# Kernel tuning notes

Measured on AMD Instinct MI355X. Metric: run time of the kernel, lower is better.

Reference implementation:

```python
import jax, jax.numpy as jnp
import numpy as np

HEAD_SIZE = 64

def setup_inputs() -> dict:
    key = jax.random.key(0)
    kx, kk, kq, kv = jax.random.split(key, 4)
    B, T, C, H = 8, 2048, 1024, HEAD_SIZE
    scale = 1.0 / np.sqrt(C)
    x = jax.random.normal(kx, (B, T, C), dtype=jnp.float32)
    # nn.Linear(n_emb, head_size, bias=False) weights, shape (head_size, n_emb)
    Wk = jax.random.normal(kk, (H, C), dtype=jnp.float32) * scale
    Wq = jax.random.normal(kq, (H, C), dtype=jnp.float32) * scale
    Wv = jax.random.normal(kv, (H, C), dtype=jnp.float32) * scale
    return {"x": x, "Wk": Wk, "Wq": Wq, "Wv": Wv}

def reference(x, Wk, Wq, Wv):
    # x: (B,T,C); W*: (H,C). Single causal self-attention head.
    H = Wk.shape[0]
    k = jnp.einsum('btc,hc->bth', x, Wk)
    q = jnp.einsum('btc,hc->bth', x, Wq)
    v = jnp.einsum('btc,hc->bth', x, Wv)
    scores = jnp.einsum('bth,bsh->bts', q, k) / jnp.sqrt(jnp.float32(H))
    T = x.shape[1]
    causal = jnp.tril(jnp.ones((T, T), dtype=bool))  # (T,T)
    scores = jnp.where(causal, scores, -jnp.inf)
    attn = jax.nn.softmax(scores, axis=-1)
    out = jnp.einsum('bts,bsh->bth', attn, v)  # (B,T,H)
    return out
```

## Files before the change

kernel.cpp:

```cpp
#include <hip/hip_runtime.h>
#include <hip/hip_bf16.h>

typedef __bf16 bf16_t;
typedef __bf16 bf16x8 __attribute__((ext_vector_type(8)));
typedef float  f32x4  __attribute__((ext_vector_type(4)));

#define B_ 8
#define T_ 2048
#define C_ 1024
#define H_ 64

#define MFMA16(a, b, c) __builtin_amdgcn_mfma_f32_16x16x32_bf16((a), (b), (c), 0, 0, 0)
#define GLL16(g, l) __builtin_amdgcn_global_load_lds( \
    (const __attribute__((address_space(1))) unsigned int*)(g), \
    (__attribute__((address_space(3))) unsigned int*)(l), 16, 0, 0)

__global__ __launch_bounds__(256) void wconv_kernel(
    const float* __restrict__ Wk, const float* __restrict__ Wq,
    const float* __restrict__ Wv,
    bf16_t* __restrict__ Wh, bf16_t* __restrict__ Wl)
{
    int i = blockIdx.x * 256 + threadIdx.x;
    int r = i >> 10;
    int c = i & 1023;
    float v;
    if (r < 64)       v = Wq[r * 1024 + c];
    else if (r < 128) v = Wk[(r - 64) * 1024 + c];
    else              v = Wv[(r - 128) * 1024 + c];
    bf16_t h = (bf16_t)v;
    Wh[i] = h;
    Wl[i] = (bf16_t)(v - (float)h);
}

__global__ __launch_bounds__(256, 2) void proj_kernel(
    const float*  __restrict__ x,
    const bf16_t* __restrict__ Wh, const bf16_t* __restrict__ Wl,
    bf16_t* __restrict__ qh, bf16_t* __restrict__ ql,
    bf16_t* __restrict__ kh, bf16_t* __restrict__ kl,
    bf16_t* __restrict__ vh)
{
    __shared__ bf16_t Wlds[2][24][512];

    const int tid   = threadIdx.x;
    const int wid   = tid >> 6;
    const int lane  = tid & 63;
    const int quad  = lane >> 4;
    const int l16   = lane & 15;
    const int mhalf = wid >> 1;
    const int nhalf = wid & 1;
    const int g     = blockIdx.x * 32 + mhalf * 16 + l16;
    const float* xrow = x + (size_t)g * C_;

    auto stage = [&](int k0, int bufi) {
        #pragma unroll
        for (int i = 0; i < 6; ++i) {
            int grp = wid * 6 + i;
            int mat = (grp >= 12);
            int nt  = mat ? grp - 12 : grp;
            const bf16_t* src = (mat ? Wl : Wh) + (nt * 16 + l16) * 1024 + k0 + quad * 8;
            GLL16(src, &Wlds[bufi][grp][0]);
        }
    };

    f32x4 x0a, x0b, x1a, x1b;
    x0a = *(const f32x4*)(xrow + quad * 8);
    x0b = *(const f32x4*)(xrow + quad * 8 + 4);
    x1a = *(const f32x4*)(xrow + 32 + quad * 8);
    x1b = *(const f32x4*)(xrow + 32 + quad * 8 + 4);
    stage(0, 0);

    f32x4 acc[6];
    #pragma unroll
    for (int i = 0; i < 6; ++i) acc[i] = (f32x4){0.f, 0.f, 0.f, 0.f};

    int buf = 0;
    for (int it = 0; it < 32; ++it) {
        float xv[8];
        *(f32x4*)xv       = x0a;
        *(f32x4*)(xv + 4) = x0b;
        x0a = x1a; x0b = x1b;

        if (it + 1 < 32) {
            stage((it + 1) * 32, buf ^ 1);
            if (it + 2 < 32) {
                x1a = *(const f32x4*)(xrow + (it + 2) * 32 + quad * 8);
                x1b = *(const f32x4*)(xrow + (it + 2) * 32 + quad * 8 + 4);
                asm volatile("s_waitcnt vmcnt(8)" ::: "memory");
            } else {
                asm volatile("s_waitcnt vmcnt(6)" ::: "memory");
            }
        } else {
            asm volatile("s_waitcnt vmcnt(0)" ::: "memory");
        }
        __syncthreads();

        bf16x8 ah, al;
        #pragma unroll
        for (int jj = 0; jj < 8; ++jj) {
            bf16_t h = (bf16_t)xv[jj];
            ah[jj] = h;
            al[jj] = (bf16_t)(xv[jj] - (float)h);
        }

        #pragma unroll
        for (int nt = 0; nt < 6; ++nt) {
            int grp = nhalf * 6 + nt;
            bf16x8 bh = *(const bf16x8*)(&Wlds[buf][grp][lane * 8]);
            bf16x8 bl = *(const bf16x8*)(&Wlds[buf][12 + grp][lane * 8]);
            acc[nt] = MFMA16(ah, bh, acc[nt]);
            acc[nt] = MFMA16(ah, bl, acc[nt]);
            acc[nt] = MFMA16(al, bh, acc[nt]);
        }

        __syncthreads();
        buf ^= 1;
    }

    const int rowbase = blockIdx.x * 32 + mhalf * 16 + quad * 4;
    for (int nt = 0; nt < 6; ++nt) {
        int n = (nhalf * 6 + nt) * 16 + l16;
        for (int rr = 0; rr < 4; ++rr) {
            int grow = rowbase + rr;
            int bb = grow >> 11, t = grow & 2047;
            float v  = acc[nt][rr];
            bf16_t h = (bf16_t)v;
            if (n < 64) {
                int off = (bb * T_ + t) * H_ + n;
                qh[off] = h; ql[off] = (bf16_t)(v - (float)h);
            } else if (n < 128) {
                int off = (bb * T_ + t) * H_ + (n - 64);
                kh[off] = h; kl[off] = (bf16_t)(v - (float)h);
            } else {
                vh[(bb * H_ + (n - 128)) * T_ + t] = h;
            }
        }
    }
}

__global__ __launch_bounds__(512, 4) void attn_kernel(
    const bf16_t* __restrict__ qh, const bf16_t* __restrict__ ql,
    const bf16_t* __restrict__ kh, const bf16_t* __restrict__ kl,
    const bf16_t* __restrict__ vh,
    float* __restrict__ Oacc, float* __restrict__ lacc)
{
    __shared__ bf16_t KV[2][3][4096];
    __shared__ bf16_t Plds[8][16 * 72];

    const int tid  = threadIdx.x;
    const int wid  = tid >> 6;
    const int lane = tid & 63;
    const int quad = lane >> 4;
    const int l16  = lane & 15;

    const int b  = blockIdx.x & 7;
    const int gp = (blockIdx.x >> 3) & 7;
    const int s  = blockIdx.x >> 6;
    const int gA = gp, gB = 15 - gp;
    const int nA = 2 * gA + 2;

    const int t_nt   = wid >> 1;
    const int t_kk   = wid & 1;
    const int t_l16  = tid & 15;
    const int t_quad = (tid >> 4) & 3;
    const int koff   = (t_nt * 16 + t_l16) * H_ + t_kk * 32 + t_quad * 8;
    const int voff   = (t_nt * 16 + t_l16) * T_ + t_kk * 32 + t_quad * 8;

    auto stage = [&](int j, int bufi) {
        const size_t kbase = (size_t)(b * T_ + 64 * j) * H_;
        GLL16(kh + kbase + koff, &KV[bufi][0][wid * 512]);
        GLL16(kl + kbase + koff, &KV[bufi][1][wid * 512]);
        GLL16(vh + (size_t)b * H_ * T_ + 64 * j + voff, &KV[bufi][2][wid * 512]);
    };

    f32x4  O[4];
    float  rowsum[4];
    bf16x8 aqh[2], aql[2];
    int    gcur = -1;

    auto flushO = [&]() {
        #pragma unroll
        for (int rr = 0; rr < 4; ++rr) {
            int trow = b * T_ + 128 * gcur + 16 * wid + quad * 4 + rr;
            #pragma unroll
            for (int ht = 0; ht < 4; ++ht)
                atomicAdd(Oacc + (size_t)trow * H_ + ht * 16 + l16, O[ht][rr]);
            float s_ = rowsum[rr];
            s_ += __shfl_xor(s_, 1, 64);
            s_ += __shfl_xor(s_, 2, 64);
            s_ += __shfl_xor(s_, 4, 64);
            s_ += __shfl_xor(s_, 8, 64);
            if (l16 == 0) atomicAdd(lacc + trow, s_);
        }
    };

    {
        int u0 = s;
        int j0 = (u0 < nA) ? u0 : (u0 - nA);
        stage(j0, 0);
    }

    int buf = 0;
    for (int u = s; u < 34; u += 8) {
        const int g = (u < nA) ? gA : gB;
        const int j = (u < nA) ? u : (u - nA);

        const int un = u + 8;
        if (un < 34) {
            int jn = (un < nA) ? un : (un - nA);
            stage(jn, buf ^ 1);
            asm volatile("s_waitcnt vmcnt(3)" ::: "memory");
        } else {
            asm volatile("s_waitcnt vmcnt(0)" ::: "memory");
        }
        __syncthreads();

        if (g != gcur) {
            if (gcur >= 0) flushO();
            gcur = g;
            const size_t qoff = (size_t)(b * T_ + 128 * g + 16 * wid + l16) * H_;
            #pragma unroll
            for (int kk = 0; kk < 2; ++kk) {
                aqh[kk] = *(const bf16x8*)(qh + qoff + kk * 32 + quad * 8);
                aql[kk] = *(const bf16x8*)(ql + qoff + kk * 32 + quad * 8);
            }
            #pragma unroll
            for (int i = 0; i < 4; ++i) { O[i] = (f32x4){0.f,0.f,0.f,0.f}; rowsum[i] = 0.f; }
        }

        const bf16_t* Kh = KV[buf][0];
        const bf16_t* Kl = KV[buf][1];
        f32x4 S[4];
        #pragma unroll
        for (int i = 0; i < 4; ++i) S[i] = (f32x4){0.f,0.f,0.f,0.f};
        #pragma unroll
        for (int nt = 0; nt < 4; ++nt) {
            #pragma unroll
            for (int kk = 0; kk < 2; ++kk) {
                bf16x8 bh = *(const bf16x8*)(Kh + (nt * 2 + kk) * 512 + lane * 8);
                bf16x8 bl = *(const bf16x8*)(Kl + (nt * 2 + kk) * 512 + lane * 8);
                S[nt] = MFMA16(aqh[kk], bh, S[nt]);
                S[nt] = MFMA16(aqh[kk], bl, S[nt]);
                S[nt] = MFMA16(aql[kk], bh, S[nt]);
            }
        }

        bf16_t* Pw = Plds[wid];
        const int rloc = 128 * g + 16 * wid + quad * 4;
        #pragma unroll
        for (int nt = 0; nt < 4; ++nt) {
            int colt = 64 * j + nt * 16 + l16;
            #pragma unroll
            for (int rr = 0; rr < 4; ++rr) {
                float pv = (colt <= rloc + rr)
                         ? __expf(fmaf(S[nt][rr], 0.125f, -20.0f)) : 0.f;
                rowsum[rr] += pv;
                Pw[(quad * 4 + rr) * 72 + nt * 16 + l16] = (bf16_t)pv;
            }
        }

        bf16x8 ap0 = *(const bf16x8*)(Pw + l16 * 72 + quad * 8);
        bf16x8 ap1 = *(const bf16x8*)(Pw + l16 * 72 + 32 + quad * 8);

        const bf16_t* Vt = KV[buf][2];
        #pragma unroll
        for (int ht = 0; ht < 4; ++ht) {
            bf16x8 bv0 = *(const bf16x8*)(Vt + (ht * 2 + 0) * 512 + lane * 8);
            bf16x8 bv1 = *(const bf16x8*)(Vt + (ht * 2 + 1) * 512 + lane * 8);
            O[ht] = MFMA16(ap0, bv0, O[ht]);
            O[ht] = MFMA16(ap1, bv1, O[ht]);
        }

        __syncthreads();
        buf ^= 1;
    }
    if (gcur >= 0) flushO();
}

__global__ __launch_bounds__(256) void div_kernel(
    const float* __restrict__ Oacc, const float* __restrict__ lacc,
    float* __restrict__ out)
{
    int i = blockIdx.x * 256 + threadIdx.x;
    f32x4 o   = ((const f32x4*)Oacc)[i];
    float inv = 1.0f / lacc[i >> 4];
    ((f32x4*)out)[i] = o * inv;
}

extern "C" void kernel_launch(void* const* d_in, const int* in_sizes, int n_in,
                              void* d_out, int out_size, void* d_ws, size_t ws_size,
                              hipStream_t stream)
{
    const float* x  = (const float*)d_in[0];
    const float* Wk = (const float*)d_in[1];
    const float* Wq = (const float*)d_in[2];
    const float* Wv = (const float*)d_in[3];
    float* out = (float*)d_out;

    char* ws = (char*)d_ws;
    const size_t WSZ = 192 * 1024 * sizeof(bf16_t);
    const size_t QSZ = (size_t)B_ * T_ * H_ * sizeof(bf16_t);
    bf16_t* Wh   = (bf16_t*)(ws);
    bf16_t* Wl   = (bf16_t*)(ws + WSZ);
    bf16_t* qh   = (bf16_t*)(ws + 2 * WSZ);
    bf16_t* ql   = (bf16_t*)(ws + 2 * WSZ + 1 * QSZ);
    bf16_t* kh   = (bf16_t*)(ws + 2 * WSZ + 2 * QSZ);
    bf16_t* kl   = (bf16_t*)(ws + 2 * WSZ + 3 * QSZ);
    bf16_t* vh   = (bf16_t*)(ws + 2 * WSZ + 4 * QSZ);
    float*  Oacc = (float*)(ws + 2 * WSZ + 5 * QSZ);
    float*  lacc = (float*)(ws + 2 * WSZ + 5 * QSZ + (size_t)B_ * T_ * H_ * 4);

    hipMemsetAsync(Oacc, 0, (size_t)B_ * T_ * H_ * 4 + (size_t)B_ * T_ * 4, stream);
    hipLaunchKernelGGL(wconv_kernel, dim3(768), dim3(256), 0, stream, Wk, Wq, Wv, Wh, Wl);
    hipLaunchKernelGGL(proj_kernel, dim3(512), dim3(256), 0, stream,
                       x, Wh, Wl, qh, ql, kh, kl, vh);
    hipLaunchKernelGGL(attn_kernel, dim3(512), dim3(512), 0, stream,
                       qh, ql, kh, kl, vh, Oacc, lacc);
    hipLaunchKernelGGL(div_kernel, dim3(1024), dim3(256), 0, stream, Oacc, lacc, out);
}
```

Before: 192.9 us.

## Enlarge projection tiles to 64 rows and fold accumulator memset into wconv

The projection kernel now uses 512-thread blocks that each cover 64 rows and 64 k-values per iteration. This halves the number of iterations and barriers, and lets each staged weight tile serve twice as many rows. The separate hipMemsetAsync that zeroed the O/l accumulators is removed; extra blocks of the weight conversion kernel now do that zeroing, saving one launch. The trade-offs are a doubled LDS footprint (about 96 KB per block), which may limit residency to one block per CU, and only 256 blocks in the projection grid.

```diff
diff --git a/kernel.cpp b/kernel.cpp
--- a/kernel.cpp
+++ b/kernel.cpp
@@ -18,28 +18,32 @@
 __global__ __launch_bounds__(256) void wconv_kernel(
     const float* __restrict__ Wk, const float* __restrict__ Wq,
     const float* __restrict__ Wv,
-    bf16_t* __restrict__ Wh, bf16_t* __restrict__ Wl)
+    bf16_t* __restrict__ Wh, bf16_t* __restrict__ Wl,
+    f32x4* __restrict__ zero_dst)
 {
     int i = blockIdx.x * 256 + threadIdx.x;
-    int r = i >> 10;
-    int c = i & 1023;
-    float v;
-    if (r < 64)       v = Wq[r * 1024 + c];
-    else if (r < 128) v = Wk[(r - 64) * 1024 + c];
-    else              v = Wv[(r - 128) * 1024 + c];
-    bf16_t h = (bf16_t)v;
-    Wh[i] = h;
-    Wl[i] = (bf16_t)(v - (float)h);
-}
-
-__global__ __launch_bounds__(256, 2) void proj_kernel(
+    zero_dst[i] = (f32x4){0.f, 0.f, 0.f, 0.f};
+    if (blockIdx.x < 768) {
+        int r = i >> 10;
+        int c = i & 1023;
+        float v;
+        if (r < 64)       v = Wq[r * 1024 + c];
+        else if (r < 128) v = Wk[(r - 64) * 1024 + c];
+        else              v = Wv[(r - 128) * 1024 + c];
+        bf16_t h = (bf16_t)v;
+        Wh[i] = h;
+        Wl[i] = (bf16_t)(v - (float)h);
+    }
+}
+
+__global__ __launch_bounds__(512, 2) void proj_kernel(
     const float*  __restrict__ x,
     const bf16_t* __restrict__ Wh, const bf16_t* __restrict__ Wl,
     bf16_t* __restrict__ qh, bf16_t* __restrict__ ql,
     bf16_t* __restrict__ kh, bf16_t* __restrict__ kl,
     bf16_t* __restrict__ vh)
 {
-    __shared__ bf16_t Wlds[2][24][512];
+    __shared__ bf16_t Wlds[2][48][512];
 
     const int tid   = threadIdx.x;
     const int wid   = tid >> 6;
@@ -48,44 +52,54 @@
     const int l16   = lane & 15;
     const int mhalf = wid >> 1;
     const int nhalf = wid & 1;
-    const int g     = blockIdx.x * 32 + mhalf * 16 + l16;
+    const int g     = blockIdx.x * 64 + mhalf * 16 + l16;
     const float* xrow = x + (size_t)g * C_;
 
     auto stage = [&](int k0, int bufi) {
         #pragma unroll
         for (int i = 0; i < 6; ++i) {
-            int grp = wid * 6 + i;
-            int mat = (grp >= 12);
-            int nt  = mat ? grp - 12 : grp;
-            const bf16_t* src = (mat ? Wl : Wh) + (nt * 16 + l16) * 1024 + k0 + quad * 8;
+            int grp  = wid * 6 + i;
+            int ksub = (grp >= 24);
+            int rem  = grp - ksub * 24;
+            int mat  = (rem >= 12);
+            int nt   = rem - mat * 12;
+            const bf16_t* src = (mat ? Wl : Wh)
+                + (nt * 16 + l16) * 1024 + k0 + ksub * 32 + quad * 8;
             GLL16(src, &Wlds[bufi][grp][0]);
         }
     };
-
-    f32x4 x0a, x0b, x1a, x1b;
-    x0a = *(const f32x4*)(xrow + quad * 8);
-    x0b = *(const f32x4*)(xrow + quad * 8 + 4);
-    x1a = *(const f32x4*)(xrow + 32 + quad * 8);
-    x1b = *(const f32x4*)(xrow + 32 + quad * 8 + 4);
+    auto loadx = [&](int it, f32x4* d) {
+        #pragma unroll
+        for (int ks = 0; ks < 2; ++ks) {
+            d[ks * 2]     = *(const f32x4*)(xrow + it * 64 + ks * 32 + quad * 8);
+            d[ks * 2 + 1] = *(const f32x4*)(xrow + it * 64 + ks * 32 + quad * 8 + 4);
+        }
+    };
+
     stage(0, 0);
+    f32x4 x0[4], x1[4];
+    loadx(0, x0);
+    loadx(1, x1);
 
     f32x4 acc[6];
     #pragma unroll
     for (int i = 0; i < 6; ++i) acc[i] = (f32x4){0.f, 0.f, 0.f, 0.f};
 
     int buf = 0;
-    for (int it = 0; it < 32; ++it) {
-        float xv[8];
-        *(f32x4*)xv       = x0a;
-        *(f32x4*)(xv + 4) = x0b;
-        x0a = x1a; x0b = x1b;
-
-        if (it + 1 < 32) {
-            stage((it + 1) * 32, buf ^ 1);
-            if (it + 2 < 32) {
-                x1a = *(const f32x4*)(xrow + (it + 2) * 32 + quad * 8);
-                x1b = *(const f32x4*)(xrow + (it + 2) * 32 + quad * 8 + 4);
-                asm volatile("s_waitcnt vmcnt(8)" ::: "memory");
+    for (int it = 0; it < 16; ++it) {
+        float xv[16];
+        *(f32x4*)(xv)      = x0[0];
+        *(f32x4*)(xv + 4)  = x0[1];
+        *(f32x4*)(xv + 8)  = x0[2];
+        *(f32x4*)(xv + 12) = x0[3];
+        #pragma unroll
+        for (int i = 0; i < 4; ++i) x0[i] = x1[i];
+
+        if (it + 1 < 16) {
+            stage((it + 1) * 64, buf ^ 1);
+            if (it + 2 < 16) {
+                loadx(it + 2, x1);
+                asm volatile("s_waitcnt vmcnt(10)" ::: "memory");
             } else {
                 asm volatile("s_waitcnt vmcnt(6)" ::: "memory");
             }
@@ -94,29 +108,32 @@
         }
         __syncthreads();
 
-        bf16x8 ah, al;
-        #pragma unroll
-        for (int jj = 0; jj < 8; ++jj) {
-            bf16_t h = (bf16_t)xv[jj];
-            ah[jj] = h;
-            al[jj] = (bf16_t)(xv[jj] - (float)h);
-        }
-
-        #pragma unroll
-        for (int nt = 0; nt < 6; ++nt) {
-            int grp = nhalf * 6 + nt;
-            bf16x8 bh = *(const bf16x8*)(&Wlds[buf][grp][lane * 8]);
-            bf16x8 bl = *(const bf16x8*)(&Wlds[buf][12 + grp][lane * 8]);
-            acc[nt] = MFMA16(ah, bh, acc[nt]);
-            acc[nt] = MFMA16(ah, bl, acc[nt]);
-            acc[nt] = MFMA16(al, bh, acc[nt]);
+        #pragma unroll
+        for (int ks = 0; ks < 2; ++ks) {
+            bf16x8 ah, al;
+            #pragma unroll
+            for (int jj = 0; jj < 8; ++jj) {
+                float  xf = xv[ks * 8 + jj];
+                bf16_t h  = (bf16_t)xf;
+                ah[jj] = h;
+                al[jj] = (bf16_t)(xf - (float)h);
+            }
+            #pragma unroll
+            for (int nt = 0; nt < 6; ++nt) {
+                int gi = ks * 24 + nhalf * 6 + nt;
+                bf16x8 bh = *(const bf16x8*)(&Wlds[buf][gi][lane * 8]);
+                bf16x8 bl = *(const bf16x8*)(&Wlds[buf][gi + 12][lane * 8]);
+                acc[nt] = MFMA16(ah, bh, acc[nt]);
+                acc[nt] = MFMA16(ah, bl, acc[nt]);
+                acc[nt] = MFMA16(al, bh, acc[nt]);
+            }
         }
 
         __syncthreads();
         buf ^= 1;
     }
 
-    const int rowbase = blockIdx.x * 32 + mhalf * 16 + quad * 4;
+    const int rowbase = blockIdx.x * 64 + mhalf * 16 + quad * 4;
     for (int nt = 0; nt < 6; ++nt) {
         int n = (nhalf * 6 + nt) * 16 + l16;
         for (int rr = 0; rr < 4; ++rr) {
@@ -309,9 +326,9 @@
     float*  Oacc = (float*)(ws + 2 * WSZ + 5 * QSZ);
     float*  lacc = (float*)(ws + 2 * WSZ + 5 * QSZ + (size_t)B_ * T_ * H_ * 4);
 
-    hipMemsetAsync(Oacc, 0, (size_t)B_ * T_ * H_ * 4 + (size_t)B_ * T_ * 4, stream);
-    hipLaunchKernelGGL(wconv_kernel, dim3(768), dim3(256), 0, stream, Wk, Wq, Wv, Wh, Wl);
-    hipLaunchKernelGGL(proj_kernel, dim3(512), dim3(256), 0, stream,
+    hipLaunchKernelGGL(wconv_kernel, dim3(1040), dim3(256), 0, stream,
+                       Wk, Wq, Wv, Wh, Wl, (f32x4*)Oacc);
+    hipLaunchKernelGGL(proj_kernel, dim3(256), dim3(512), 0, stream,
                        x, Wh, Wl, qh, ql, kh, kl, vh);
     hipLaunchKernelGGL(attn_kernel, dim3(512), dim3(512), 0, stream,
                        qh, ql, kh, kl, vh, Oacc, lacc);
```

After: 184.7 us. -4.3%, faster.

## Fuse workspace zeroing into weight conversion, widen projection blocks, use raw barriers

Applied to the files above, without the earlier changes.

Removes the separate memset by having the weight-conversion kernel also zero the Oacc/lacc accumulators through extra blocks. The projection kernel now uses 512-thread blocks with 8 waves, each handling 3 output tiles instead of 6. This halves per-wave accumulators and staging, which raises occupancy and latency hiding. __syncthreads is replaced with a bare s_barrier to avoid the implicit waitcnt. That relies on the explicit vmcnt waits for correctness and could expose LDS hazards.

```diff
diff --git a/kernel.cpp b/kernel.cpp
--- a/kernel.cpp
+++ b/kernel.cpp
@@ -14,25 +14,30 @@
 #define GLL16(g, l) __builtin_amdgcn_global_load_lds( \
     (const __attribute__((address_space(1))) unsigned int*)(g), \
     (__attribute__((address_space(3))) unsigned int*)(l), 16, 0, 0)
+#define SBAR() asm volatile("s_barrier" ::: "memory")
 
 __global__ __launch_bounds__(256) void wconv_kernel(
     const float* __restrict__ Wk, const float* __restrict__ Wq,
     const float* __restrict__ Wv,
-    bf16_t* __restrict__ Wh, bf16_t* __restrict__ Wl)
+    bf16_t* __restrict__ Wh, bf16_t* __restrict__ Wl,
+    f32x4* __restrict__ zero_dst)
 {
     int i = blockIdx.x * 256 + threadIdx.x;
-    int r = i >> 10;
-    int c = i & 1023;
-    float v;
-    if (r < 64)       v = Wq[r * 1024 + c];
-    else if (r < 128) v = Wk[(r - 64) * 1024 + c];
-    else              v = Wv[(r - 128) * 1024 + c];
-    bf16_t h = (bf16_t)v;
-    Wh[i] = h;
-    Wl[i] = (bf16_t)(v - (float)h);
-}
-
-__global__ __launch_bounds__(256, 2) void proj_kernel(
+    zero_dst[i] = (f32x4){0.f, 0.f, 0.f, 0.f};
+    if (blockIdx.x < 768) {
+        int r = i >> 10;
+        int c = i & 1023;
+        float v;
+        if (r < 64)       v = Wq[r * 1024 + c];
+        else if (r < 128) v = Wk[(r - 64) * 1024 + c];
+        else              v = Wv[(r - 128) * 1024 + c];
+        bf16_t h = (bf16_t)v;
+        Wh[i] = h;
+        Wl[i] = (bf16_t)(v - (float)h);
+    }
+}
+
+__global__ __launch_bounds__(512, 4) void proj_kernel(
     const float*  __restrict__ x,
     const bf16_t* __restrict__ Wh, const bf16_t* __restrict__ Wl,
     bf16_t* __restrict__ qh, bf16_t* __restrict__ ql,
@@ -46,53 +51,54 @@
     const int lane  = tid & 63;
     const int quad  = lane >> 4;
     const int l16   = lane & 15;
-    const int mhalf = wid >> 1;
-    const int nhalf = wid & 1;
+    const int mhalf = wid >> 2;
+    const int nq    = wid & 3;
     const int g     = blockIdx.x * 32 + mhalf * 16 + l16;
     const float* xrow = x + (size_t)g * C_;
 
     auto stage = [&](int k0, int bufi) {
         #pragma unroll
-        for (int i = 0; i < 6; ++i) {
-            int grp = wid * 6 + i;
+        for (int i = 0; i < 3; ++i) {
+            int grp = wid * 3 + i;
             int mat = (grp >= 12);
-            int nt  = mat ? grp - 12 : grp;
+            int nt  = grp - mat * 12;
             const bf16_t* src = (mat ? Wl : Wh) + (nt * 16 + l16) * 1024 + k0 + quad * 8;
             GLL16(src, &Wlds[bufi][grp][0]);
         }
     };
-
-    f32x4 x0a, x0b, x1a, x1b;
-    x0a = *(const f32x4*)(xrow + quad * 8);
-    x0b = *(const f32x4*)(xrow + quad * 8 + 4);
-    x1a = *(const f32x4*)(xrow + 32 + quad * 8);
-    x1b = *(const f32x4*)(xrow + 32 + quad * 8 + 4);
+    auto loadx = [&](int it, f32x4* d) {
+        d[0] = *(const f32x4*)(xrow + it * 32 + quad * 8);
+        d[1] = *(const f32x4*)(xrow + it * 32 + quad * 8 + 4);
+    };
+
     stage(0, 0);
-
-    f32x4 acc[6];
+    f32x4 x0[2], x1[2];
+    loadx(0, x0);
+    loadx(1, x1);
+
+    f32x4 acc[3];
     #pragma unroll
-    for (int i = 0; i < 6; ++i) acc[i] = (f32x4){0.f, 0.f, 0.f, 0.f};
+    for (int i = 0; i < 3; ++i) acc[i] = (f32x4){0.f, 0.f, 0.f, 0.f};
 
     int buf = 0;
     for (int it = 0; it < 32; ++it) {
         float xv[8];
-        *(f32x4*)xv       = x0a;
-        *(f32x4*)(xv + 4) = x0b;
-        x0a = x1a; x0b = x1b;
+        *(f32x4*)(xv)     = x0[0];
+        *(f32x4*)(xv + 4) = x0[1];
+        x0[0] = x1[0]; x0[1] = x1[1];
 
         if (it + 1 < 32) {
             stage((it + 1) * 32, buf ^ 1);
             if (it + 2 < 32) {
-                x1a = *(const f32x4*)(xrow + (it + 2) * 32 + quad * 8);
-                x1b = *(const f32x4*)(xrow + (it + 2) * 32 + quad * 8 + 4);
-                asm volatile("s_waitcnt vmcnt(8)" ::: "memory");
+                loadx(it + 2, x1);
+                asm volatile("s_waitcnt vmcnt(5)" ::: "memory");
             } else {
-                asm volatile("s_waitcnt vmcnt(6)" ::: "memory");
+                asm volatile("s_waitcnt vmcnt(3)" ::: "memory");
             }
         } else {
             asm volatile("s_waitcnt vmcnt(0)" ::: "memory");
         }
-        __syncthreads();
+        SBAR();
 
         bf16x8 ah, al;
         #pragma unroll
@@ -103,22 +109,22 @@
         }
 
         #pragma unroll
-        for (int nt = 0; nt < 6; ++nt) {
-            int grp = nhalf * 6 + nt;
-            bf16x8 bh = *(const bf16x8*)(&Wlds[buf][grp][lane * 8]);
-            bf16x8 bl = *(const bf16x8*)(&Wlds[buf][12 + grp][lane * 8]);
+        for (int nt = 0; nt < 3; ++nt) {
+            int gi = nq * 3 + nt;
+            bf16x8 bh = *(const bf16x8*)(&Wlds[buf][gi][lane * 8]);
+            bf16x8 bl = *(const bf16x8*)(&Wlds[buf][gi + 12][lane * 8]);
             acc[nt] = MFMA16(ah, bh, acc[nt]);
             acc[nt] = MFMA16(ah, bl, acc[nt]);
             acc[nt] = MFMA16(al, bh, acc[nt]);
         }
 
-        __syncthreads();
+        SBAR();
         buf ^= 1;
     }
 
     const int rowbase = blockIdx.x * 32 + mhalf * 16 + quad * 4;
-    for (int nt = 0; nt < 6; ++nt) {
-        int n = (nhalf * 6 + nt) * 16 + l16;
+    for (int nt = 0; nt < 3; ++nt) {
+        int n = (nq * 3 + nt) * 16 + l16;
         for (int rr = 0; rr < 4; ++rr) {
             int grow = rowbase + rr;
             int bb = grow >> 11, t = grow & 2047;
@@ -212,7 +218,7 @@
         } else {
             asm volatile("s_waitcnt vmcnt(0)" ::: "memory");
         }
-        __syncthreads();
+        SBAR();
 
         if (g != gcur) {
             if (gcur >= 0) flushO();
@@ -270,7 +276,7 @@
             O[ht] = MFMA16(ap1, bv1, O[ht]);
         }
 
-        __syncthreads();
+        SBAR();
         buf ^= 1;
     }
     if (gcur >= 0) flushO();
@@ -309,9 +315,9 @@
     float*  Oacc = (float*)(ws + 2 * WSZ + 5 * QSZ);
     float*  lacc = (float*)(ws + 2 * WSZ + 5 * QSZ + (size_t)B_ * T_ * H_ * 4);
 
-    hipMemsetAsync(Oacc, 0, (size_t)B_ * T_ * H_ * 4 + (size_t)B_ * T_ * 4, stream);
-    hipLaunchKernelGGL(wconv_kernel, dim3(768), dim3(256), 0, stream, Wk, Wq, Wv, Wh, Wl);
-    hipLaunchKernelGGL(proj_kernel, dim3(512), dim3(256), 0, stream,
+    hipLaunchKernelGGL(wconv_kernel, dim3(1040), dim3(256), 0, stream,
+                       Wk, Wq, Wv, Wh, Wl, (f32x4*)Oacc);
+    hipLaunchKernelGGL(proj_kernel, dim3(512), dim3(512), 0, stream,
                        x, Wh, Wl, qh, ql, kh, kl, vh);
     hipLaunchKernelGGL(attn_kernel, dim3(512), dim3(512), 0, stream,
                        qh, ql, kh, kl, vh, Oacc, lacc);
```

Result: slower. 197.6 us (+2.4%).
